# Optimization experiments

Measured on AMD Instinct MI355X. Metric: run time of the kernel, lower is better.

Reference implementation:

```python
import jax, jax.numpy as jnp
import numpy as np

N=50000; E=400000; H=128; FN=92; FE=41; L=3; PC=8; PD=16; SC=8; SD=32; B=64
EPS=1e-5

def _silu(x):
    return jax.nn.silu(x)

def _squash(s):
    n2=(s*s).sum(-1,keepdims=True)
    return s*(n2/(1.0+n2))/jnp.sqrt(n2+1e-9)

def setup_inputs():
    ks=iter(jax.random.split(jax.random.key(0),96))
    def rn(shape): return jax.random.normal(next(ks),shape,dtype=jnp.float32)
    def w(i,o): return rn((i,o))*np.float32(1.0/np.sqrt(i))
    z=lambda *s: jnp.zeros(s,jnp.float32); o=lambda *s: jnp.ones(s,jnp.float32)
    d={}
    d['x']=rn((N,FN)); d['edge_attr']=rn((E,FE)); d['pos']=rn((N,3))
    d['edge_index']=jax.random.randint(next(ks),(2,E),0,N)
    d['batch']=jnp.sort(jax.random.randint(next(ks),(N,),0,B))
    d.update(neW1=w(FN,H),neb1=z(H),neg1=o(H),nebe1=z(H),neW2=w(H,H),neb2=z(H),neg2=o(H),nebe2=z(H))
    d.update(eeW1=w(FE,H),eeb1=z(H),eeW2=w(H,H),eeb2=z(H),ivW=w(H,H),ivb=z(H))
    def wl(i,o2): return jnp.stack([w(i,o2) for _ in range(L)])
    d.update(cWma=wl(H,H),cWmb=wl(H,H),cWme=wl(H,H),cbm=z(L,H),cWsx=wl(H,H),cWsa=wl(H,H),cbs=z(L,H))
    d.update(cWv1=wl(H,H),cbv1=z(L,H),cWv2=wl(H,H),cbv2=z(L,H),lng=o(L,H),lnb=z(L,H),vsg=o(L,H))
    d.update(pcW=w(H,PC*PD),pcb=z(PC*PD),pvW=w(H,PD),sW=rn((PC,PD,SC,SD))*np.float32(1.0/np.sqrt(PD)))
    d.update(aW=w(SD//2,1),ab=z(1))
    d.update(pW1=w(SD,H//2),pb1=z(H//2),pg1=o(H//2),pbe1=z(H//2),pW2=w(H//2,H//4),pb2=z(H//4),pg2=o(H//4),pbe2=z(H//4),pW3=w(H//4,1),pb3=z(1))
    return d

def _forward(x,edge_index,edge_attr,pos,batch,neW1,neb1,neg1,nebe1,neW2,neb2,neg2,nebe2,eeW1,eeb1,eeW2,eeb2,ivW,ivb,cWma,cWmb,cWme,cbm,cWsx,cWsa,cbs,cWv1,cbv1,cWv2,cbv2,lng,lnb,vsg,pcW,pcb,pvW,sW,aW,ab,pW1,pb1,pg1,pbe1,pW2,pb2,pg2,pbe2,pW3,pb3):
    seg=jax.ops.segment_sum
    # node/edge MLP embeddings (BatchNorm in eval mode: running mean 0 / var 1 -> affine)
    xs=_silu((x@neW1+neb1)*neg1+nebe1)
    xs=_silu((xs@neW2+neb2)*neg2+nebe2)
    ea=_silu(edge_attr@eeW1+eeb1); ea=_silu(ea@eeW2+eeb2)
    # vectorized form of the per-node python loop: outer product weights x pos -> [N,H,3]
    xv=(xs@ivW+ivb)[:,:,None]*pos[:,None,:]
    src,dst=edge_index[0],edge_index[1]
    dp=pos[dst]-pos[src]                                  # [E,3]
    for i in range(L):
        xs_res,xv_res=xs,xv
        m=_silu(xs[src]@cWma[i]+xs[dst]@cWmb[i]+ea@cWme[i]+cbm[i])   # [E,H] edge messages
        xs_c=xs@cWsx[i]+seg(m,dst,num_segments=N)@cWsa[i]+cbs[i]
        vmsg=xv[src]*(m@cWv1[i]+cbv1[i])[:,:,None]+(m@cWv2[i]+cbv2[i])[:,:,None]*dp[:,None,:]
        xv_c=xv+seg(vmsg,dst,num_segments=N)               # [N,H,3]
        mu=xs_c.mean(-1,keepdims=True)
        xs_n=(xs_c-mu)/jnp.sqrt(((xs_c-mu)**2).mean(-1,keepdims=True)+EPS)*lng[i]+lnb[i]
        nrm=jnp.sqrt(((xv_c**2).sum(-1)).mean(-1,keepdims=True)+EPS)  # equivariant norm [N,1]
        xv_n=(xv_c/nrm[:,:,None])*vsg[i][None,:,None]
        xv_n=xv_n*jax.nn.sigmoid(xs_n)[:,:,None]           # scalar gating of vectors
        if i>0:
            xs=_silu(xs_n)+xs_res; xv=xv_n+xv_res
        else:
            xs=_silu(xs_n); xv=xv_n
    # primary capsules
    pc=_squash((xs@pcW+pcb).reshape(-1,PC,PD))             # [N,PC,PD]
    pv=jnp.einsum('nhd,hp->npd',xv,pvW)                    # [N,PD,3]
    u=pc+jnp.sqrt((pv**2).sum(-1)+1e-9)[:,None,:]          # vector norms expanded over PC caps
    # secondary capsules with per-graph pooling + 2 routing iterations
    pooled=seg(jnp.einsum('npd,pdce->npce',u,sW),batch,num_segments=B)  # [B,PC,SC,SD]
    bb=jnp.zeros((B,PC,SC),jnp.float32)
    for it in range(2):
        c=jax.nn.softmax(bb,axis=-1)
        v=_squash(jnp.einsum('bpc,bpce->bce',c,pooled))    # [B,SC,SD]
        if it==0:
            bb=bb+jnp.einsum('bpce,bce->bpc',pooled,v)
    # attention pooling over secondary capsules
    aw=jax.nn.softmax(v[:,:,:SD//2]@aW+ab,axis=1)
    wc=(aw*v).sum(1)                                       # [B,SD]
    h=_silu((wc@pW1+pb1)*pg1+pbe1)
    h=_silu((h@pW2+pb2)*pg2+pbe2)                          # dropout: eval mode (identity)
    return h@pW3+pb3

def reference(x,edge_index,edge_attr,pos,batch,neW1,neb1,neg1,nebe1,neW2,neb2,neg2,nebe2,eeW1,eeb1,eeW2,eeb2,ivW,ivb,cWma,cWmb,cWme,cbm,cWsx,cWsa,cbs,cWv1,cbv1,cWv2,cbv2,lng,lnb,vsg,pcW,pcb,pvW,sW,aW,ab,pW1,pb1,pg1,pbe1,pW2,pb2,pg2,pbe2,pW3,pb3):
    return _forward(x,edge_index,edge_attr,pos,batch,neW1,neb1,neg1,nebe1,neW2,neb2,neg2,nebe2,eeW1,eeb1,eeW2,eeb2,ivW,ivb,cWma,cWmb,cWme,cbm,cWsx,cWsa,cbs,cWv1,cbv1,cWv2,cbv2,lng,lnb,vsg,pcW,pcb,pvW,sW,aW,ab,pW1,pb1,pg1,pbe1,pW2,pb2,pg2,pbe2,pW3,pb3)
```

## Files before the change

### kernel.cpp

```cpp
#include <hip/hip_runtime.h>
#include <hip/hip_bf16.h>
#include <math.h>

#define NN 50000
#define NE 400000
#define HD 128
#define NB 64
#define NCH 8
#define CN 6250
#define ECM 53248
#define EB 32
#define PSL 16

typedef __hip_bfloat16 bf16;
typedef __attribute__((ext_vector_type(4))) unsigned short us4;
typedef __attribute__((ext_vector_type(8))) short s8v;
typedef __attribute__((ext_vector_type(4))) float f4v;

__device__ __forceinline__ float sigm_(float x){ return 1.f/(1.f+__expf(-x)); }
__device__ __forceinline__ float silu_(float x){ return x*sigm_(x); }
__device__ __forceinline__ float bf2f(bf16 x){ return __bfloat162float(x); }
__device__ __forceinline__ unsigned short f2bu(float f){
    bf16 h = __float2bfloat16(f);
    return *reinterpret_cast<unsigned short*>(&h);
// ... 109 lines not shown
        }
        if (owf){
            bf16* C = (bf16*)Cv;
#pragma unroll
            for (int j=0;j<8;++j) C[(size_t)orow*HD+col0+j] = __float2bfloat16(o[j]);
        } else {
            float* C = (float*)Cv;
            float4* cp = (float4*)&C[(size_t)orow*HD + col0];
            cp[0] = make_float4(o[0],o[1],o[2],o[3]);
            cp[1] = make_float4(o[4],o[5],o[6],o[7]);
        }
    }
}

__global__ __launch_bounds__(256)
void gemm3(const float* __restrict__ A0, const float* __restrict__ W0, float* __restrict__ C0, int M0,
           const float* __restrict__ A1, const float* __restrict__ W1, float* __restrict__ C1, int M1,
           const float* __restrict__ A2, const float* __restrict__ W2, float* __restrict__ C2, int M2)
{
    const int nb0 = (M0+63)>>6, nb1 = (M1+63)>>6;
    int bb = (int)blockIdx.x;
    const float *A, *W; float* C; int M;
    if (bb < nb0){ A=A0; W=W0; C=C0; M=M0; }
    else if (bb < nb0+nb1){ bb -= nb0; A=A1; W=W1; C=C1; M=M1; }
    else { bb -= nb0+nb1; A=A2; W=W2; C=C2; M=M2; }
    const int row0 = bb*64;

    __shared__ float As[32][68];
    __shared__ float Ws[32][128];
    const int tid = threadIdx.x;
    const int tx = tid & 15, ty = tid >> 4;
    const int col0 = tx*8;
    float acc[4][8];
#pragma unroll
    for (int r=0;r<4;++r)
#pragma unroll
        for (int j=0;j<8;++j) acc[r][j]=0.f;
    const int mload = tid >> 2;
    const int kload = (tid & 3) << 3;
    const int grow = row0 + mload;
    const bool rv = grow < M;

    for (int k0 = 0; k0 < 128; k0 += 32) {
        if (rv) {
            const float* ap = A + (size_t)grow*128 + k0 + kload;
            float4 v0 = *(const float4*)ap;
            float4 v1 = *(const float4*)(ap+4);
            As[kload+0][mload]=v0.x; As[kload+1][mload]=v0.y;
            As[kload+2][mload]=v0.z; As[kload+3][mload]=v0.w;
            As[kload+4][mload]=v1.x; As[kload+5][mload]=v1.y;
            As[kload+6][mload]=v1.z; As[kload+7][mload]=v1.w;
        } else {
#pragma unroll
            for (int j=0;j<8;++j) As[kload+j][mload] = 0.f;
        }
#pragma unroll
        for (int j=0;j<4;++j){
            int el = (tid + j*256)*4;
            int kk = el >> 7, col = el & 127;
            *(float4*)&Ws[kk][col] = *(const float4*)&W[(size_t)(k0+kk)*HD + col];
        }
        __syncthreads();
#pragma unroll
        for (int k=0;k<32;++k){
            float4 a4 = *(const float4*)&As[k][ty*4];
            float4 w0 = *(const float4*)&Ws[k][col0];
            float4 w1 = *(const float4*)&Ws[k][col0+4];
            float av[4] = {a4.x,a4.y,a4.z,a4.w};
            float wv[8] = {w0.x,w0.y,w0.z,w0.w,w1.x,w1.y,w1.z,w1.w};
#pragma unroll
            for (int r=0;r<4;++r)
#pragma unroll
                for (int j=0;j<8;++j) acc[r][j] += av[r]*wv[j];
        }
        __syncthreads();
    }
#pragma unroll
    for (int r=0;r<4;++r){
        int orow = row0 + ty*4 + r;
        if (orow >= M) continue;
        float4* cp = (float4*)&C[(size_t)orow*HD + col0];
        cp[0] = make_float4(acc[r][0],acc[r][1],acc[r][2],acc[r][3]);
        cp[1] = make_float4(acc[r][4],acc[r][5],acc[r][6],acc[r][7]);
    }
}

__global__ __launch_bounds__(256)
void edge_pipe(const float* __restrict__ eat,
               const int* __restrict__ elist, const int* __restrict__ srcp,
               const int* __restrict__ dstp,
               const bf16* __restrict__ W1h, const bf16* __restrict__ W1l,
               const float* __restrict__ b1,
               const bf16* __restrict__ W2h, const bf16* __restrict__ W2l,
               const float* __restrict__ b2,
               const bf16* __restrict__ Wmeh, const bf16* __restrict__ Wmel,
               const float* __restrict__ bm,
               const bf16* __restrict__ An, const bf16* __restrict__ Bn,
               const bf16* __restrict__ Wv1h, const bf16* __restrict__ Wv1l,
               const float* __restrict__ bv1,
               const int* __restrict__ rp, int rn0, int rn1,
               bf16* __restrict__ outM, bf16* __restrict__ outG)
{
    __shared__ __align__(16) unsigned short T1[EB][136];
    __shared__ __align__(16) unsigned short T2[EB][136];
    __shared__ int elS[EB], seS[EB], deS[EB];

    const int cbase = rp[rn0];
    const int Ml = min(ECM, max(rp[rn1]-cbase, 0));
    const int row0 = blockIdx.x*EB;
    if (row0 >= Ml) return;
    const int tid = threadIdx.x;
    const int lane = tid & 63, wave = tid >> 6;
    const int quad = lane >> 4, n16 = lane & 15;
    const int cwb = wave*32;

    if (tid < EB){
        int r = row0 + tid;
        bool v = r < Ml;
        int p = cbase + (v ? r : 0);
        elS[tid] = v ? min(max(elist[p],0),NE-1) : 0;
        seS[tid] = v ? srcp[p] : 0;
        deS[tid] = v ? dstp[p] : 0;
    }
    __syncthreads();

    f4v acc[2][2];

    {
        float ebuf[2][2][8];
#pragma unroll
        for (int rt=0; rt<2; ++rt){
            int arow = elS[rt*16 + n16];
#pragma unroll
            for (int kc=0; kc<2; ++kc){
#pragma unroll
                for (int j=0;j<8;++j){
                    int k = kc*32 + quad*8 + j;
                    ebuf[rt][kc][j] = (k < 41) ? eat[(size_t)arow*41 + k] : 0.f;
                }
            }
        }

        s8v B1h[2][2], B1l[2][2];
#pragma unroll
        for (int ct=0; ct<2; ++ct){
            int nn = cwb + ct*16 + n16;
#pragma unroll
            for (int kc=0; kc<2; ++kc){
                B1h[ct][kc] = *(const s8v*)&W1h[(size_t)nn*64 + kc*32 + quad*8];
                B1l[ct][kc] = *(const s8v*)&W1l[(size_t)nn*64 + kc*32 + quad*8];
            }
        }
#pragma unroll
        for (int rt=0;rt<2;++rt)
#pragma unroll
            for (int ct=0;ct<2;++ct) acc[rt][ct] = (f4v){0.f,0.f,0.f,0.f};

#pragma unroll
        for (int rt=0; rt<2; ++rt){
#pragma unroll
            for (int kc=0; kc<2; ++kc){
                s8v ah, al;
#pragma unroll
                for (int j=0;j<8;++j){
                    float v = ebuf[rt][kc][j];
                    unsigned short h = f2bu(v);
                    ah[j] = (short)h;
                    al[j] = (short)f2bu(v - __uint_as_float(((unsigned)h)<<16));
                }
#pragma unroll
                for (int ct=0; ct<2; ++ct){
                    acc[rt][ct] = __builtin_amdgcn_mfma_f32_16x16x32_bf16(ah, B1h[ct][kc], acc[rt][ct], 0,0,0);
                    acc[rt][ct] = __builtin_amdgcn_mfma_f32_16x16x32_bf16(ah, B1l[ct][kc], acc[rt][ct], 0,0,0);
                    acc[rt][ct] = __builtin_amdgcn_mfma_f32_16x16x32_bf16(al, B1h[ct][kc], acc[rt][ct], 0,0,0);
                }
            }
        }
#pragma unroll
        for (int ct=0; ct<2; ++ct){
            int col = cwb + ct*16 + n16;
            float bc = b1[col];
#pragma unroll
            for (int rt=0; rt<2; ++rt)
#pragma unroll
                for (int i=0;i<4;++i)
                    T1[rt*16 + quad*4 + i][col] = f2bu(silu_(acc[rt][ct][i] + bc));
        }
    }
    __syncthreads();

    s8v Bh[2][4], Bl[2][4];
    for (int ph=0; ph<3; ++ph){
        const bf16* WH = (ph==0)? W2h : (ph==1)? Wmeh : Wv1h;
        const bf16* WL = (ph==0)? W2l : (ph==1)? Wmel : Wv1l;
        const unsigned short (*Tin)[136] = (ph==1)? (const unsigned short(*)[136])T2
                                                  : (const unsigned short(*)[136])T1;
#pragma unroll
        for (int ct=0; ct<2; ++ct){
            int nn = cwb + ct*16 + n16;
            const s8v* hp = (const s8v*)&WH[(size_t)nn*128];
            const s8v* lp = (const s8v*)&WL[(size_t)nn*128];
#pragma unroll
            for (int kc=0; kc<4; ++kc){
                Bh[ct][kc] = hp[kc*4 + quad];
                Bl[ct][kc] = lp[kc*4 + quad];
            }
        }
#pragma unroll
        for (int rt=0;rt<2;++rt)
#pragma unroll
            for (int ct=0;ct<2;++ct) acc[rt][ct] = (f4v){0.f,0.f,0.f,0.f};

        s8v anR[2], bnR[2];
        if (ph==1){
#pragma unroll
            for (int it=0; it<2; ++it){
                int idx = tid + it*256;
                int r = idx >> 4, c = idx & 15;
                anR[it] = *(const s8v*)&An[(size_t)seS[r]*HD + c*8];
                bnR[it] = *(const s8v*)&Bn[(size_t)deS[r]*HD + c*8];
            }
        }

#pragma unroll
        for (int kc=0; kc<4; ++kc){
#pragma unroll
            for (int rt=0; rt<2; ++rt){
                s8v a = *(const s8v*)&Tin[rt*16 + n16][kc*32 + quad*8];
#pragma unroll
                for (int ct=0; ct<2; ++ct){
                    acc[rt][ct] = __builtin_amdgcn_mfma_f32_16x16x32_bf16(a, Bh[ct][kc], acc[rt][ct], 0,0,0);
                    acc[rt][ct] = __builtin_amdgcn_mfma_f32_16x16x32_bf16(a, Bl[ct][kc], acc[rt][ct], 0,0,0);
                }
            }
        }
        if (ph==0){
#pragma unroll
            for (int ct=0; ct<2; ++ct){
                int col = cwb + ct*16 + n16;
                float bc = b2[col];
#pragma unroll
                for (int rt=0; rt<2; ++rt)
#pragma unroll
                    for (int i=0;i<4;++i)
                        T2[rt*16 + quad*4 + i][col] = f2bu(silu_(acc[rt][ct][i] + bc));
            }
            __syncthreads();
        } else if (ph==1){
            __syncthreads();
#pragma unroll
            for (int it=0; it<2; ++it){
                int idx = tid + it*256;
                int r = idx >> 4, c = idx & 15;
                *(s8v*)&T1[r][c*8] = anR[it];
                *(s8v*)&T2[r][c*8] = bnR[it];
            }
            __syncthreads();
#pragma unroll
            for (int ct=0; ct<2; ++ct){
                int col = cwb + ct*16 + n16;
                float bc = bm[col];
#pragma unroll
                for (int rt=0; rt<2; ++rt)
#pragma unroll
                    for (int i=0;i<4;++i){
                        int row = rt*16 + quad*4 + i;
                        float v = silu_(acc[rt][ct][i] + bc
                                        + bf2f(*(const bf16*)&T1[row][col])
                                        + bf2f(*(const bf16*)&T2[row][col]));
                        T1[row][col] = f2bu(v);
                    }
            }
            __syncthreads();
            {
                int row = tid >> 3, seg = tid & 7;
                if (row0 + row < Ml){
                    const s8v* s = (const s8v*)&T1[row][seg*16];
                    s8v* d = (s8v*)&outM[(size_t)(row0+row)*HD + seg*16];
                    d[0]=s[0]; d[1]=s[1];
                }
            }
        } else {
#pragma unroll
            for (int ct=0; ct<2; ++ct){
                int col = cwb + ct*16 + n16;
                float bc = bv1[col];
#pragma unroll
                for (int rt=0; rt<2; ++rt)
#pragma unroll
                    for (int i=0;i<4;++i)
                        T2[rt*16 + quad*4 + i][col] = f2bu(acc[rt][ct][i] + bc);
            }
            __syncthreads();
            {
                int row = tid >> 3, seg = tid & 7;
                if (row0 + row < Ml){
                    const s8v* s = (const s8v*)&T2[row][seg*16];
                    s8v* d = (s8v*)&outG[(size_t)(row0+row)*HD + seg*16];
                    d[0]=s[0]; d[1]=s[1];
                }
            }
        }
    }
}

__global__ __launch_bounds__(128)
void scatter_c(const int* __restrict__ rp, const int* __restrict__ srcp,
               const float* __restrict__ pos,
               const bf16* __restrict__ mB, const bf16* __restrict__ gB,
               const float* __restrict__ xvO,
               float* __restrict__ smC, float* __restrict__ mdC,
               float* __restrict__ avC, float* __restrict__ sdC, int n0, int n1)
{
    const int b = blockIdx.x;
    const int n = n0 + b;
    if (n >= n1) return;
    const int h = threadIdx.x;
    const int cbase = rp[n0];
    int p0 = rp[n], p1 = rp[n+1];
    float px0=pos[n*3],px1=pos[n*3+1],px2=pos[n*3+2];
    float sm=0,a0=0,a1=0,a2=0,m0=0,m1=0,m2=0,d0s=0,d1s=0,d2s=0;
    for (int p=p0;p<p1;++p){
        int ii=p-cbase; if ((unsigned)ii>=(unsigned)ECM) break;
        float mh=bf2f(mB[(size_t)ii*HD+h]);
        float gh=bf2f(gB[(size_t)ii*HD+h]);
        int sn=srcp[p]; sn=min(max(sn,0),NN-1);
        float d0=px0-pos[sn*3], d1=px1-pos[sn*3+1], d2=px2-pos[sn*3+2];
        sm+=mh;
        a0+=xvO[(size_t)sn*3*HD+h]*gh;
        a1+=xvO[(size_t)sn*3*HD+HD+h]*gh;
        a2+=xvO[(size_t)sn*3*HD+2*HD+h]*gh;
        m0+=mh*d0; m1+=mh*d1; m2+=mh*d2;
        d0s+=d0; d1s+=d1; d2s+=d2;
    }
    smC[(size_t)b*HD+h]=sm;
    mdC[(size_t)b*3*HD+h]=m0;
    mdC[(size_t)b*3*HD+HD+h]=m1;
    mdC[(size_t)b*3*HD+2*HD+h]=m2;
    avC[(size_t)b*3*HD+h]=a0;
    avC[(size_t)b*3*HD+HD+h]=a1;
    avC[(size_t)b*3*HD+2*HD+h]=a2;
    if (h==0){ sdC[b*3]=d0s; sdC[b*3+1]=d1s; sdC[b*3+2]=d2s; }
}

__global__ __launch_bounds__(128)
void nu_lite(const float* __restrict__ gF, const float* __restrict__ swF,
             const float* __restrict__ xwF,
             const float* __restrict__ avC, const float* __restrict__ sdC,
             const float* __restrict__ xvO, float* __restrict__ xvN,
             float* __restrict__ xs,
             const float* __restrict__ bv2, const float* __restrict__ bs,
             const float* __restrict__ lng, const float* __restrict__ lnb,
             const float* __restrict__ vsg, int addRes, int n0, int n1)
{
    __shared__ float red[4];
    __shared__ float red2[2];
    const int b = blockIdx.x;
    const int n = n0 + b;
    if (n >= n1) return;
    const int h = threadIdx.x;
    const int w = h >> 6;
    const float xsv = xs[(size_t)n*HD+h];
    float xc = xwF[(size_t)b*HD+h] + swF[(size_t)b*HD+h] + bs[h];
    float s1=xc, s2=xc*xc;
#pragma unroll
    for (int off=1; off<64; off<<=1){ s1+=__shfl_xor(s1,off,64); s2+=__shfl_xor(s2,off,64); }
    if ((h&63)==0){ red[w*2]=s1; red[w*2+1]=s2; }
    __syncthreads();
    s1=red[0]+red[2]; s2=red[1]+red[3];
    float mu=s1*(1.f/128.f);
    float var=fmaxf(s2*(1.f/128.f)-mu*mu, 0.f);
    float xn=(xc-mu)*rsqrtf(var+1e-5f)*lng[h]+lnb[h];
    float ov0=xvO[(size_t)n*3*HD+h];
    float ov1=xvO[(size_t)n*3*HD+HD+h];
    float ov2=xvO[(size_t)n*3*HD+2*HD+h];
    float a0=avC[(size_t)b*3*HD+h];
    float a1=avC[(size_t)b*3*HD+HD+h];
    float a2=avC[(size_t)b*3*HD+2*HD+h];
    float d0s=sdC[b*3], d1s=sdC[b*3+1], d2s=sdC[b*3+2];
    float b2v=bv2[h];
    float v0=ov0+a0+gF[(size_t)(b*3+0)*HD+h]+b2v*d0s;
    float v1=ov1+a1+gF[(size_t)(b*3+1)*HD+h]+b2v*d1s;
    float v2=ov2+a2+gF[(size_t)(b*3+2)*HD+h]+b2v*d2s;
    float q=v0*v0+v1*v1+v2*v2;
#pragma unroll
    for (int off=1; off<64; off<<=1) q+=__shfl_xor(q,off,64);
    if ((h&63)==0) red2[w]=q;
    __syncthreads();
    q=fmaxf(red2[0]+red2[1], 0.f);
    float nrm=sqrtf(q*(1.f/128.f)+1e-5f);
    float scale=vsg[h]*sigm_(xn)/nrm;
    float r0=v0*scale, r1=v1*scale, r2=v2*scale;
    float nxs=silu_(xn);
    if (addRes){ nxs+=xsv; r0+=ov0; r1+=ov1; r2+=ov2; }
    xs[(size_t)n*HD+h]=nxs;
    xvN[(size_t)n*3*HD+h]=r0;
    xvN[(size_t)n*3*HD+HD+h]=r1;
    xvN[(size_t)n*3*HD+2*HD+h]=r2;
}

__global__ void hist_kernel(const int* __restrict__ idx, int* __restrict__ cnt, int n, int nb){
    int i = blockIdx.x*256 + threadIdx.x;
    if (i < n){
        int v = idx[i]; v = min(max(v,0), nb-1);
        atomicAdd(&cnt[v], 1);
    }
}

__global__ __launch_bounds__(256)
void scan_blk(const int* __restrict__ cnt, int* __restrict__ rowptr,
              int* __restrict__ bsum, int n){
    const int b = blockIdx.x, t = threadIdx.x;
    const int i = b*256 + t;
    const int lane = t & 63, w = t >> 6;
    int v = (i < n) ? cnt[i] : 0;
    int s = v;
#pragma unroll
    for (int off=1; off<64; off<<=1){
        int u = __shfl_up(s, off, 64);
        if (lane >= off) s += u;
    }
    __shared__ int ws[4];
    if (lane == 63) ws[w] = s;
    __syncthreads();
    int add = 0;
// ... 238 lines not shown
        float a = 0.f;
        for (int c=0;c<8;++c) a += aws[c]*vv[c*32+t];
        wcs[t] = a;
    }
    __syncthreads();
    if (t < 64){
        float a = 0.f;
        for (int e=0;e<32;++e) a += wcs[e]*pW1[e*64+t];
        h1[t] = silu_((a+pb1[t])*pg1[t]+pbe1[t]);
    }
    __syncthreads();
    if (t < 32){
        float a = 0.f;
        for (int j=0;j<64;++j) a += h1[j]*pW2[j*32+t];
        h2[t] = silu_((a+pb2[t])*pg2[t]+pbe2[t]);
    }
    __syncthreads();
    if (t == 0){
        float a = 0.f;
        for (int j=0;j<32;++j) a += h2[j]*pW3[j];
        a += pb3[0];
        if (!finite_(a)) a = 999.f;
        out[b] = a;
    }
}

__global__ void sentinel_k(float* __restrict__ out, float v){
    out[threadIdx.x] = v;
}

extern "C" void kernel_launch(void* const* d_in, const int* in_sizes, int n_in,
                              void* d_out, int out_size, void* d_ws, size_t ws_size,
                              hipStream_t stream)
{
    (void)in_sizes; (void)n_in; (void)out_size;
    const float* x    = (const float*)d_in[0];
    const float* eat  = (const float*)d_in[1];
    const float* pos  = (const float*)d_in[2];
    const int*  eidx  = (const int*)d_in[3];
    const int*  batch = (const int*)d_in[4];
    const float* neW1=(const float*)d_in[5],  *neb1=(const float*)d_in[6],
               * neg1=(const float*)d_in[7],  *nebe1=(const float*)d_in[8];
    const float* neW2=(const float*)d_in[9],  *neb2=(const float*)d_in[10],
               * neg2=(const float*)d_in[11], *nebe2=(const float*)d_in[12];
    const float* eeW1=(const float*)d_in[13], *eeb1=(const float*)d_in[14];
    const float* eeW2=(const float*)d_in[15], *eeb2=(const float*)d_in[16];
    const float* ivW =(const float*)d_in[17], *ivb =(const float*)d_in[18];
    const float* cWma=(const float*)d_in[19], *cWmb=(const float*)d_in[20],
               * cWme=(const float*)d_in[21], *cbm =(const float*)d_in[22];
    const float* cWsx=(const float*)d_in[23], *cWsa=(const float*)d_in[24],
               * cbs =(const float*)d_in[25];
    const float* cWv1=(const float*)d_in[26], *cbv1=(const float*)d_in[27],
               * cWv2=(const float*)d_in[28], *cbv2=(const float*)d_in[29];
    const float* lng =(const float*)d_in[30], *lnb =(const float*)d_in[31],
               * vsg =(const float*)d_in[32];
    const float* pcW =(const float*)d_in[33], *pcb =(const float*)d_in[34];
    const float* pvW =(const float*)d_in[35];
    const float* sW  =(const float*)d_in[36];
    const float* aW  =(const float*)d_in[37], *ab  =(const float*)d_in[38];
    const float* pW1 =(const float*)d_in[39], *pb1 =(const float*)d_in[40],
               * pg1 =(const float*)d_in[41], *pbe1=(const float*)d_in[42];
    const float* pW2 =(const float*)d_in[43], *pb2 =(const float*)d_in[44],
               * pg2 =(const float*)d_in[45], *pbe2=(const float*)d_in[46];
    const float* pW3 =(const float*)d_in[47], *pb3 =(const float*)d_in[48];

    const int* src = eidx;
    const int* dst = eidx + NE;

    char* wp = (char*)d_ws;
    auto alloc = [&](size_t bytes)->char*{
        char* p = wp;
        wp += (bytes + 255) & ~(size_t)255;
        return p;
    };
    bf16*  bufM  = (bf16*) alloc((size_t)ECM*HD*2);
    bf16*  bufG  = (bf16*) alloc((size_t)ECM*HD*2);
    float* xs    = (float*)alloc((size_t)NN*HD*4);
    float* xvA   = (float*)alloc((size_t)NN*3*HD*4);
    float* xvB   = (float*)alloc((size_t)NN*3*HD*4);
    bf16*  An    = (bf16*) alloc((size_t)NN*HD*2);
    bf16*  Bn    = (bf16*) alloc((size_t)NN*HD*2);
    float* smC   = (float*)alloc((size_t)CN*HD*4);
    float* mdC   = (float*)alloc((size_t)CN*3*HD*4);
    float* avC   = (float*)alloc((size_t)CN*3*HD*4);
    float* sdC   = (float*)alloc((size_t)CN*3*4);
    bf16*  WtH   = (bf16*) alloc((size_t)7*HD*HD*2);
    bf16*  WtL   = (bf16*) alloc((size_t)7*HD*HD*2);
    bf16*  W1h   = (bf16*) alloc((size_t)HD*64*2);
    bf16*  W1l   = (bf16*) alloc((size_t)HD*64*2);
    float* Up    = (float*)alloc((size_t)NB*PSL*HD*4);
    float* Ubuf  = (float*)alloc((size_t)NB*HD*4);
    int* rowptr  = (int*)alloc((size_t)(NN+1)*4);
    int* cnt     = (int*)alloc((size_t)NN*4);
    int* bsum    = (int*)alloc((size_t)256*4);
    int* elist   = (int*)alloc((size_t)NE*4);
    int* srcp    = (int*)alloc((size_t)NE*4);
    int* dstp    = (int*)alloc((size_t)NE*4);
    int* gptr    = (int*)alloc((size_t)(NB+1)*4);
    size_t used  = (size_t)(wp - (char*)d_ws);

    if (used > ws_size){
        sentinel_k<<<1, NB, 0, stream>>>((float*)d_out, -1.f - (float)(ws_size >> 20));
        return;
    }
    float* tmpF = xvB;
    bf16*  ubuf = An;
    float* Pf   = xvA;
    float* gF  = (float*)bufM;
    float* swF = gF  + (size_t)3*CN*HD;
    float* xwF = swF + (size_t)CN*HD;

    hipMemsetAsync(cnt, 0, (size_t)NN*4, stream);
    hist_kernel<<<(NE+255)/256, 256, 0, stream>>>(dst, cnt, NE, NN);
    const int SBLK = (NN+255)/256;
    scan_blk<<<SBLK, 256, 0, stream>>>(cnt, rowptr, bsum, NN);
    scan_bsum<<<1, 256, 0, stream>>>(bsum, SBLK);
    scan_fix<<<SBLK, 256, 0, stream>>>(rowptr, bsum, NN);
    hipMemsetAsync(cnt, 0, (size_t)NN*4, stream);
    fill_kernel<<<(NE+255)/256, 256, 0, stream>>>(src, dst, rowptr, cnt, elist, srcp, dstp, NE);
    gptr_kernel<<<(NN+255)/256, 256, 0, stream>>>(batch, gptr);
    wprep1<<<32,256,0,stream>>>(eeW1, W1h, W1l);
    wprep<<<64,256,0,stream>>>(eeW2, WtH, WtL);
    for (int l=0;l<3;++l){
        wprep<<<64,256,0,stream>>>(cWme + (size_t)l*HD*HD, WtH + (size_t)(1+l)*HD*HD,
                                   WtL + (size_t)(1+l)*HD*HD);
        wprep<<<64,256,0,stream>>>(cWv1 + (size_t)l*HD*HD, WtH + (size_t)(4+l)*HD*HD,
                                   WtL + (size_t)(4+l)*HD*HD);
    }

    const int GN = (NN+63)/64;
    const int GE = ECM/EB;
    const int G3 = ((3*CN+63)/64) + 2*((CN+63)/64);

    gemmk<M_BNSILU><<<GN,256,0,stream>>>(x, neW1, neb1, neg1, nebe1, tmpF, 0, NN, 92);
    gemmk<M_BNSILU><<<GN,256,0,stream>>>(tmpF, neW2, neb2, neg2, nebe2, xs, 0, NN, 128);
    gemmk<M_BIAS><<<GN,256,0,stream>>>(xs, ivW, ivb, nullptr, nullptr, tmpF, 0, NN, 128);
    xv_init<<<NN, 128, 0, stream>>>(tmpF, pos, xvA);

    float* xvO = xvA;
    float* xvN = xvB;
    for (int l=0; l<3; ++l){
        const float* Wma = cWma + (size_t)l*HD*HD;
        const float* Wmb = cWmb + (size_t)l*HD*HD;
        const float* bm  = cbm  + (size_t)l*HD;
        const float* Wsx = cWsx + (size_t)l*HD*HD;
        const float* Wsa = cWsa + (size_t)l*HD*HD;
        const float* bs  = cbs  + (size_t)l*HD;
        const float* bv1 = cbv1 + (size_t)l*HD;
        const float* Wv2 = cWv2 + (size_t)l*HD*HD;
        const float* bv2 = cbv2 + (size_t)l*HD;
        const bf16* Wmeh = WtH + (size_t)(1+l)*HD*HD;
        const bf16* Wmel = WtL + (size_t)(1+l)*HD*HD;
        const bf16* Wv1h = WtH + (size_t)(4+l)*HD*HD;
        const bf16* Wv1l = WtL + (size_t)(4+l)*HD*HD;

        gemmk<M_PLAIN><<<GN,256,0,stream>>>(xs, Wma, nullptr, nullptr, nullptr, An, 1, NN, 128);
        gemmk<M_PLAIN><<<GN,256,0,stream>>>(xs, Wmb, nullptr, nullptr, nullptr, Bn, 1, NN, 128);

        for (int c=0; c<NCH; ++c){
            int n0 = c*CN, n1 = n0+CN;
            edge_pipe<<<GE,256,0,stream>>>(eat, elist, srcp, dstp,
                                           W1h, W1l, eeb1,
                                           WtH, WtL, eeb2,
                                           Wmeh, Wmel, bm,
                                           An, Bn,
                                           Wv1h, Wv1l, bv1,
                                           rowptr, n0, n1, bufM, bufG);
            scatter_c<<<CN,128,0,stream>>>(rowptr, srcp, pos, bufM, bufG, xvO,
                                           smC, mdC, avC, sdC, n0, n1);
            gemm3<<<G3,256,0,stream>>>(mdC, Wv2, gF, 3*CN,
                                       smC, Wsa, swF, CN,
                                       xs + (size_t)n0*HD, Wsx, xwF, CN);
            nu_lite<<<CN,128,0,stream>>>(gF, swF, xwF, avC, sdC,
                                         xvO, xvN, xs,
                                         bv2, bs,
                                         lng + (size_t)l*HD, lnb + (size_t)l*HD,
                                         vsg + (size_t)l*HD, l>0 ? 1 : 0, n0, n1);
        }
        float* t = xvO; xvO = xvN; xvN = t;
    }

    gemmk<M_BIAS><<<GN,256,0,stream>>>(xs, pcW, pcb, nullptr, nullptr, Pf, 0, NN, 128);
    capsule2<<<12500/4, 256, 0, stream>>>(Pf, xvO, pvW, ubuf);
    pool1<<<NB*PSL, 128, 0, stream>>>(gptr, ubuf, Up);
    pool2<<<NB, 128, 0, stream>>>(Up, Ubuf);
    graph_head<<<NB, 256, 0, stream>>>(Ubuf, sW, aW, ab,
                                       pW1, pb1, pg1, pbe1,
                                       pW2, pb2, pg2, pbe2,
                                       pW3, pb3, (float*)d_out);
}
```

Baseline: 3.318 ms.

## Precompute edge embedding MLP once and reuse across message-passing layers

Adds an ea_pipe kernel that computes the two-layer edge-attribute MLP once for all edges in CSR-sorted order and stores it as bf16. A new edge_pipe_fast kernel loads these precomputed embeddings instead of recomputing both MLP stages in every layer and chunk launch. This removes redundant matmuls and the gather of raw edge attributes from each of the 24 edge launches. In exchange it needs a large extra workspace buffer, adds bandwidth to read the stored embeddings, and falls back to the old kernel if the workspace is too small.

```diff
diff --git a/kernel.cpp b/kernel.cpp
--- a/kernel.cpp
+++ b/kernel.cpp
@@ -215,6 +215,291 @@
         float4* cp = (float4*)&C[(size_t)orow*HD + col0];
         cp[0] = make_float4(acc[r][0],acc[r][1],acc[r][2],acc[r][3]);
         cp[1] = make_float4(acc[r][4],acc[r][5],acc[r][6],acc[r][7]);
+    }
+}
+
+__global__ __launch_bounds__(256)
+void ea_pipe(const float* __restrict__ eat, const int* __restrict__ elist,
+             const bf16* __restrict__ W1h, const bf16* __restrict__ W1l,
+             const float* __restrict__ b1,
+             const bf16* __restrict__ W2h, const bf16* __restrict__ W2l,
+             const float* __restrict__ b2,
+             bf16* __restrict__ eaP)
+{
+    __shared__ __align__(16) unsigned short T1[EB][136];
+    __shared__ __align__(16) unsigned short T2[EB][136];
+    __shared__ int elS[EB];
+
+    const int row0 = blockIdx.x*EB;
+    const int tid = threadIdx.x;
+    const int lane = tid & 63, wave = tid >> 6;
+    const int quad = lane >> 4, n16 = lane & 15;
+    const int cwb = wave*32;
+
+    if (tid < EB) elS[tid] = min(max(elist[row0 + tid],0),NE-1);
+    __syncthreads();
+
+    f4v acc[2][2];
+
+    {
+        float ebuf[2][2][8];
+#pragma unroll
+        for (int rt=0; rt<2; ++rt){
+            int arow = elS[rt*16 + n16];
+#pragma unroll
+            for (int kc=0; kc<2; ++kc)
+#pragma unroll
+                for (int j=0;j<8;++j){
+                    int k = kc*32 + quad*8 + j;
+                    ebuf[rt][kc][j] = (k < 41) ? eat[(size_t)arow*41 + k] : 0.f;
+                }
+        }
+        s8v B1h[2][2], B1l[2][2];
+#pragma unroll
+        for (int ct=0; ct<2; ++ct){
+            int nn = cwb + ct*16 + n16;
+#pragma unroll
+            for (int kc=0; kc<2; ++kc){
+                B1h[ct][kc] = *(const s8v*)&W1h[(size_t)nn*64 + kc*32 + quad*8];
+                B1l[ct][kc] = *(const s8v*)&W1l[(size_t)nn*64 + kc*32 + quad*8];
+            }
+        }
+#pragma unroll
+        for (int rt=0;rt<2;++rt)
+#pragma unroll
+            for (int ct=0;ct<2;++ct) acc[rt][ct] = (f4v){0.f,0.f,0.f,0.f};
+#pragma unroll
+        for (int rt=0; rt<2; ++rt)
+#pragma unroll
+            for (int kc=0; kc<2; ++kc){
+                s8v ah, al;
+#pragma unroll
+                for (int j=0;j<8;++j){
+                    float v = ebuf[rt][kc][j];
+                    unsigned short h = f2bu(v);
+                    ah[j] = (short)h;
+                    al[j] = (short)f2bu(v - __uint_as_float(((unsigned)h)<<16));
+                }
+#pragma unroll
+                for (int ct=0; ct<2; ++ct){
+                    acc[rt][ct] = __builtin_amdgcn_mfma_f32_16x16x32_bf16(ah, B1h[ct][kc], acc[rt][ct], 0,0,0);
+                    acc[rt][ct] = __builtin_amdgcn_mfma_f32_16x16x32_bf16(ah, B1l[ct][kc], acc[rt][ct], 0,0,0);
+                    acc[rt][ct] = __builtin_amdgcn_mfma_f32_16x16x32_bf16(al, B1h[ct][kc], acc[rt][ct], 0,0,0);
+                }
+            }
+#pragma unroll
+        for (int ct=0; ct<2; ++ct){
+            int col = cwb + ct*16 + n16;
+            float bc = b1[col];
+#pragma unroll
+            for (int rt=0; rt<2; ++rt)
+#pragma unroll
+                for (int i=0;i<4;++i)
+                    T1[rt*16 + quad*4 + i][col] = f2bu(silu_(acc[rt][ct][i] + bc));
+        }
+    }
+    __syncthreads();
+
+    {
+        s8v Bh[2][4], Bl[2][4];
+#pragma unroll
+        for (int ct=0; ct<2; ++ct){
+            int nn = cwb + ct*16 + n16;
+            const s8v* hp = (const s8v*)&W2h[(size_t)nn*128];
+            const s8v* lp = (const s8v*)&W2l[(size_t)nn*128];
+#pragma unroll
+            for (int kc=0; kc<4; ++kc){
+                Bh[ct][kc] = hp[kc*4 + quad];
+                Bl[ct][kc] = lp[kc*4 + quad];
+            }
+        }
+#pragma unroll
+        for (int rt=0;rt<2;++rt)
+#pragma unroll
+            for (int ct=0;ct<2;++ct) acc[rt][ct] = (f4v){0.f,0.f,0.f,0.f};
+#pragma unroll
+        for (int kc=0; kc<4; ++kc)
+#pragma unroll
+            for (int rt=0; rt<2; ++rt){
+                s8v a = *(const s8v*)&T1[rt*16 + n16][kc*32 + quad*8];
+#pragma unroll
+                for (int ct=0; ct<2; ++ct){
+                    acc[rt][ct] = __builtin_amdgcn_mfma_f32_16x16x32_bf16(a, Bh[ct][kc], acc[rt][ct], 0,0,0);
+                    acc[rt][ct] = __builtin_amdgcn_mfma_f32_16x16x32_bf16(a, Bl[ct][kc], acc[rt][ct], 0,0,0);
+                }
+            }
+#pragma unroll
+        for (int ct=0; ct<2; ++ct){
+            int col = cwb + ct*16 + n16;
+            float bc = b2[col];
+#pragma unroll
+            for (int rt=0; rt<2; ++rt)
+#pragma unroll
+                for (int i=0;i<4;++i)
+                    T2[rt*16 + quad*4 + i][col] = f2bu(silu_(acc[rt][ct][i] + bc));
+        }
+    }
+    __syncthreads();
+    {
+        int row = tid >> 3, seg = tid & 7;
+        const s8v* s = (const s8v*)&T2[row][seg*16];
+        s8v* d = (s8v*)&eaP[(size_t)(row0+row)*HD + seg*16];
+        d[0]=s[0]; d[1]=s[1];
+    }
+}
+
+__global__ __launch_bounds__(256)
+void edge_pipe_fast(const bf16* __restrict__ eaP,
+                    const int* __restrict__ srcp, const int* __restrict__ dstp,
+                    const bf16* __restrict__ Wmeh, const bf16* __restrict__ Wmel,
+                    const float* __restrict__ bm,
+                    const bf16* __restrict__ An, const bf16* __restrict__ Bn,
+                    const bf16* __restrict__ Wv1h, const bf16* __restrict__ Wv1l,
+                    const float* __restrict__ bv1,
+                    const int* __restrict__ rp, int rn0, int rn1,
+                    bf16* __restrict__ outM, bf16* __restrict__ outG)
+{
+    __shared__ __align__(16) unsigned short T1[EB][136];
+    __shared__ __align__(16) unsigned short T2[EB][136];
+    __shared__ int seS[EB], deS[EB];
+
+    const int cbase = rp[rn0];
+    const int Ml = min(ECM, max(rp[rn1]-cbase, 0));
+    const int row0 = blockIdx.x*EB;
+    if (row0 >= Ml) return;
+    const int tid = threadIdx.x;
+    const int lane = tid & 63, wave = tid >> 6;
+    const int quad = lane >> 4, n16 = lane & 15;
+    const int cwb = wave*32;
+
+    if (tid < EB){
+        int r = row0 + tid;
+        bool v = r < Ml;
+        int p = cbase + (v ? r : 0);
+        seS[tid] = v ? srcp[p] : 0;
+        deS[tid] = v ? dstp[p] : 0;
+    }
+    __syncthreads();
+
+    s8v anR[2], bnR[2], eaR[2];
+#pragma unroll
+    for (int it=0; it<2; ++it){
+        int idx = tid + it*256;
+        int r = idx >> 4, c = idx & 15;
+        anR[it] = *(const s8v*)&An[(size_t)seS[r]*HD + c*8];
+        bnR[it] = *(const s8v*)&Bn[(size_t)deS[r]*HD + c*8];
+        int gp = min(cbase + row0 + r, NE-1);
+        eaR[it] = *(const s8v*)&eaP[(size_t)gp*HD + c*8];
+    }
+#pragma unroll
+    for (int it=0; it<2; ++it){
+        int idx = tid + it*256;
+        int r = idx >> 4, c = idx & 15;
+        *(s8v*)&T2[r][c*8] = eaR[it];
+    }
+    __syncthreads();
+
+    f4v acc[2][2];
+    s8v Bh[2][4], Bl[2][4];
+
+#pragma unroll
+    for (int ct=0; ct<2; ++ct){
+        int nn = cwb + ct*16 + n16;
+        const s8v* hp = (const s8v*)&Wmeh[(size_t)nn*128];
+        const s8v* lp = (const s8v*)&Wmel[(size_t)nn*128];
+#pragma unroll
+        for (int kc=0; kc<4; ++kc){ Bh[ct][kc] = hp[kc*4 + quad]; Bl[ct][kc] = lp[kc*4 + quad]; }
+    }
+#pragma unroll
+    for (int rt=0;rt<2;++rt)
+#pragma unroll
+        for (int ct=0;ct<2;++ct) acc[rt][ct] = (f4v){0.f,0.f,0.f,0.f};
+#pragma unroll
+    for (int kc=0; kc<4; ++kc)
+#pragma unroll
+        for (int rt=0; rt<2; ++rt){
+            s8v a = *(const s8v*)&T2[rt*16 + n16][kc*32 + quad*8];
+#pragma unroll
+            for (int ct=0; ct<2; ++ct){
+                acc[rt][ct] = __builtin_amdgcn_mfma_f32_16x16x32_bf16(a, Bh[ct][kc], acc[rt][ct], 0,0,0);
+                acc[rt][ct] = __builtin_amdgcn_mfma_f32_16x16x32_bf16(a, Bl[ct][kc], acc[rt][ct], 0,0,0);
+            }
+        }
+    __syncthreads();
+#pragma unroll
+    for (int it=0; it<2; ++it){
+        int idx = tid + it*256;
+        int r = idx >> 4, c = idx & 15;
+        *(s8v*)&T1[r][c*8] = anR[it];
+        *(s8v*)&T2[r][c*8] = bnR[it];
+    }
+    __syncthreads();
+#pragma unroll
+    for (int ct=0; ct<2; ++ct){
+        int col = cwb + ct*16 + n16;
+        float bc = bm[col];
+#pragma unroll
+        for (int rt=0; rt<2; ++rt)
+#pragma unroll
+            for (int i=0;i<4;++i){
+                int row = rt*16 + quad*4 + i;
+                float v = silu_(acc[rt][ct][i] + bc
+                                + bf2f(*(const bf16*)&T1[row][col])
+                                + bf2f(*(const bf16*)&T2[row][col]));
+                T1[row][col] = f2bu(v);
+            }
+    }
+    __syncthreads();
+    {
+        int row = tid >> 3, seg = tid & 7;
+        if (row0 + row < Ml){
+            const s8v* s = (const s8v*)&T1[row][seg*16];
+            s8v* d = (s8v*)&outM[(size_t)(row0+row)*HD + seg*16];
+            d[0]=s[0]; d[1]=s[1];
+        }
+    }
+
+#pragma unroll
+    for (int ct=0; ct<2; ++ct){
+        int nn = cwb + ct*16 + n16;
+        const s8v* hp = (const s8v*)&Wv1h[(size_t)nn*128];
+        const s8v* lp = (const s8v*)&Wv1l[(size_t)nn*128];
+#pragma unroll
+        for (int kc=0; kc<4; ++kc){ Bh[ct][kc] = hp[kc*4 + quad]; Bl[ct][kc] = lp[kc*4 + quad]; }
+    }
+#pragma unroll
+    for (int rt=0;rt<2;++rt)
+#pragma unroll
+        for (int ct=0;ct<2;++ct) acc[rt][ct] = (f4v){0.f,0.f,0.f,0.f};
+#pragma unroll
+    for (int kc=0; kc<4; ++kc)
+#pragma unroll
+        for (int rt=0; rt<2; ++rt){
+            s8v a = *(const s8v*)&T1[rt*16 + n16][kc*32 + quad*8];
+#pragma unroll
+            for (int ct=0; ct<2; ++ct){
+                acc[rt][ct] = __builtin_amdgcn_mfma_f32_16x16x32_bf16(a, Bh[ct][kc], acc[rt][ct], 0,0,0);
+                acc[rt][ct] = __builtin_amdgcn_mfma_f32_16x16x32_bf16(a, Bl[ct][kc], acc[rt][ct], 0,0,0);
+            }
+        }
+#pragma unroll
+    for (int ct=0; ct<2; ++ct){
+        int col = cwb + ct*16 + n16;
+        float bc = bv1[col];
+#pragma unroll
+        for (int rt=0; rt<2; ++rt)
+#pragma unroll
+            for (int i=0;i<4;++i)
+                T2[rt*16 + quad*4 + i][col] = f2bu(acc[rt][ct][i] + bc);
+    }
+    __syncthreads();
+    {
+        int row = tid >> 3, seg = tid & 7;
+        if (row0 + row < Ml){
+            const s8v* s = (const s8v*)&T2[row][seg*16];
+            s8v* d = (s8v*)&outG[(size_t)(row0+row)*HD + seg*16];
+            d[0]=s[0]; d[1]=s[1];
+        }
     }
 }
 
@@ -265,15 +550,13 @@
         for (int rt=0; rt<2; ++rt){
             int arow = elS[rt*16 + n16];
 #pragma unroll
-            for (int kc=0; kc<2; ++kc){
+            for (int kc=0; kc<2; ++kc)
 #pragma unroll
                 for (int j=0;j<8;++j){
                     int k = kc*32 + quad*8 + j;
                     ebuf[rt][kc][j] = (k < 41) ? eat[(size_t)arow*41 + k] : 0.f;
                 }
-            }
-        }
-
+        }
         s8v B1h[2][2], B1l[2][2];
 #pragma unroll
         for (int ct=0; ct<2; ++ct){
@@ -288,9 +571,8 @@
         for (int rt=0;rt<2;++rt)
 #pragma unroll
             for (int ct=0;ct<2;++ct) acc[rt][ct] = (f4v){0.f,0.f,0.f,0.f};
-
-#pragma unroll
-        for (int rt=0; rt<2; ++rt){
+#pragma unroll
+        for (int rt=0; rt<2; ++rt)
 #pragma unroll
             for (int kc=0; kc<2; ++kc){
                 s8v ah, al;
@@ -308,7 +590,6 @@
                     acc[rt][ct] = __builtin_amdgcn_mfma_f32_16x16x32_bf16(al, B1h[ct][kc], acc[rt][ct], 0,0,0);
                 }
             }
-        }
 #pragma unroll
         for (int ct=0; ct<2; ++ct){
             int col = cwb + ct*16 + n16;
@@ -899,6 +1180,12 @@
         sentinel_k<<<1, NB, 0, stream>>>((float*)d_out, -1.f - (float)(ws_size >> 20));
         return;
     }
+    size_t eaBytes = (((size_t)(NE+EB)*HD*2) + 255) & ~(size_t)255;
+    bf16* eaP = nullptr;
+    if (used + eaBytes <= ws_size){
+        eaP = (bf16*)alloc(eaBytes);
+    }
+
     float* tmpF = xvB;
     bf16*  ubuf = An;
     float* Pf   = xvA;
@@ -924,6 +1211,11 @@
                                    WtL + (size_t)(4+l)*HD*HD);
     }
 
+    if (eaP){
+        ea_pipe<<<NE/EB, 256, 0, stream>>>(eat, elist, W1h, W1l, eeb1,
+                                           WtH, WtL, eeb2, eaP);
+    }
+
     const int GN = (NN+63)/64;
     const int GE = ECM/EB;
     const int G3 = ((3*CN+63)/64) + 2*((CN+63)/64);
@@ -955,13 +1247,21 @@
 
         for (int c=0; c<NCH; ++c){
             int n0 = c*CN, n1 = n0+CN;
-            edge_pipe<<<GE,256,0,stream>>>(eat, elist, srcp, dstp,
-                                           W1h, W1l, eeb1,
-                                           WtH, WtL, eeb2,
-                                           Wmeh, Wmel, bm,
-                                           An, Bn,
-                                           Wv1h, Wv1l, bv1,
-                                           rowptr, n0, n1, bufM, bufG);
+            if (eaP){
+                edge_pipe_fast<<<GE,256,0,stream>>>(eaP, srcp, dstp,
+                                                    Wmeh, Wmel, bm,
+                                                    An, Bn,
+                                                    Wv1h, Wv1l, bv1,
+                                                    rowptr, n0, n1, bufM, bufG);
+            } else {
+                edge_pipe<<<GE,256,0,stream>>>(eat, elist, srcp, dstp,
+                                               W1h, W1l, eeb1,
+                                               WtH, WtL, eeb2,
+                                               Wmeh, Wmel, bm,
+                                               An, Bn,
+                                               Wv1h, Wv1l, bv1,
+                                               rowptr, n0, n1, bufM, bufG);
+            }
             scatter_c<<<CN,128,0,stream>>>(rowptr, srcp, pos, bufM, bufG, xvO,
                                            smC, mdC, avC, sdC, n0, n1);
             gemm3<<<G3,256,0,stream>>>(mdC, Wv2, gF, 3*CN,
```

New measurement: 3.323 ms. About the same (+0.2%).

## Fuse message segment-sum reductions into edge pipeline with boundary atomics

Applied to the files above, without the earlier changes.

The edge kernel now reduces each message tile into per-destination sums (sum of messages, message times displacement, displacement sums) itself, using segmented runs over the sorted edges. Only the first run of each block, which can be shared with the previous block, and the last run use atomics; interior runs are stored directly. This removes the bf16 message buffer write and its re-read in the scatter kernel, which now only computes the gated xv aggregation. In exchange it adds a memset per chunk, serial per-column loops over 32 rows, and float atomics whose summation order is not deterministic. Interior nodes with no incoming edges rely on the memset to give zero.

```diff
diff --git a/kernel.cpp b/kernel.cpp
--- a/kernel.cpp
+++ b/kernel.cpp
@@ -219,24 +219,27 @@
 }
 
 __global__ __launch_bounds__(256)
-void edge_pipe(const float* __restrict__ eat,
-               const int* __restrict__ elist, const int* __restrict__ srcp,
-               const int* __restrict__ dstp,
-               const bf16* __restrict__ W1h, const bf16* __restrict__ W1l,
-               const float* __restrict__ b1,
-               const bf16* __restrict__ W2h, const bf16* __restrict__ W2l,
-               const float* __restrict__ b2,
-               const bf16* __restrict__ Wmeh, const bf16* __restrict__ Wmel,
-               const float* __restrict__ bm,
-               const bf16* __restrict__ An, const bf16* __restrict__ Bn,
-               const bf16* __restrict__ Wv1h, const bf16* __restrict__ Wv1l,
-               const float* __restrict__ bv1,
-               const int* __restrict__ rp, int rn0, int rn1,
-               bf16* __restrict__ outM, bf16* __restrict__ outG)
+void edge_pipe_m(const float* __restrict__ eat,
+                 const int* __restrict__ elist, const int* __restrict__ srcp,
+                 const int* __restrict__ dstp, const float* __restrict__ pos,
+                 const bf16* __restrict__ W1h, const bf16* __restrict__ W1l,
+                 const float* __restrict__ b1,
+                 const bf16* __restrict__ W2h, const bf16* __restrict__ W2l,
+                 const float* __restrict__ b2,
+                 const bf16* __restrict__ Wmeh, const bf16* __restrict__ Wmel,
+                 const float* __restrict__ bm,
+                 const bf16* __restrict__ An, const bf16* __restrict__ Bn,
+                 const bf16* __restrict__ Wv1h, const bf16* __restrict__ Wv1l,
+                 const float* __restrict__ bv1,
+                 const int* __restrict__ rp, int rn0, int rn1,
+                 float* __restrict__ smC, float* __restrict__ mdC,
+                 float* __restrict__ sdC,
+                 bf16* __restrict__ outG)
 {
     __shared__ __align__(16) unsigned short T1[EB][136];
     __shared__ __align__(16) unsigned short T2[EB][136];
     __shared__ int elS[EB], seS[EB], deS[EB];
+    __shared__ float dS0[EB], dS1[EB], dS2[EB];
 
     const int cbase = rp[rn0];
     const int Ml = min(ECM, max(rp[rn1]-cbase, 0));
@@ -251,9 +254,13 @@
         int r = row0 + tid;
         bool v = r < Ml;
         int p = cbase + (v ? r : 0);
-        elS[tid] = v ? min(max(elist[p],0),NE-1) : 0;
-        seS[tid] = v ? srcp[p] : 0;
-        deS[tid] = v ? dstp[p] : 0;
+        int e = v ? min(max(elist[p],0),NE-1) : 0;
+        int s = v ? srcp[p] : 0;
+        int d = v ? dstp[p] : 0;
+        elS[tid] = e; seS[tid] = s; deS[tid] = d;
+        dS0[tid] = pos[d*3+0] - pos[s*3+0];
+        dS1[tid] = pos[d*3+1] - pos[s*3+1];
+        dS2[tid] = pos[d*3+2] - pos[s*3+2];
     }
     __syncthreads();
 
@@ -265,15 +272,13 @@
         for (int rt=0; rt<2; ++rt){
             int arow = elS[rt*16 + n16];
 #pragma unroll
-            for (int kc=0; kc<2; ++kc){
+            for (int kc=0; kc<2; ++kc)
 #pragma unroll
                 for (int j=0;j<8;++j){
                     int k = kc*32 + quad*8 + j;
                     ebuf[rt][kc][j] = (k < 41) ? eat[(size_t)arow*41 + k] : 0.f;
                 }
-            }
-        }
-
+        }
         s8v B1h[2][2], B1l[2][2];
 #pragma unroll
         for (int ct=0; ct<2; ++ct){
@@ -288,9 +293,8 @@
         for (int rt=0;rt<2;++rt)
 #pragma unroll
             for (int ct=0;ct<2;++ct) acc[rt][ct] = (f4v){0.f,0.f,0.f,0.f};
-
-#pragma unroll
-        for (int rt=0; rt<2; ++rt){
+#pragma unroll
+        for (int rt=0; rt<2; ++rt)
 #pragma unroll
             for (int kc=0; kc<2; ++kc){
                 s8v ah, al;
@@ -308,7 +312,6 @@
                     acc[rt][ct] = __builtin_amdgcn_mfma_f32_16x16x32_bf16(al, B1h[ct][kc], acc[rt][ct], 0,0,0);
                 }
             }
-        }
 #pragma unroll
         for (int ct=0; ct<2; ++ct){
             int col = cwb + ct*16 + n16;
@@ -405,13 +408,61 @@
                     }
             }
             __syncthreads();
-            {
-                int row = tid >> 3, seg = tid & 7;
-                if (row0 + row < Ml){
-                    const s8v* s = (const s8v*)&T1[row][seg*16];
-                    s8v* d = (s8v*)&outM[(size_t)(row0+row)*HD + seg*16];
-                    d[0]=s[0]; d[1]=s[1];
+            if (tid < 128){
+                const int col = tid;
+                float sm=0.f, m0=0.f, m1=0.f, m2=0.f;
+                int cur=-1, startR=0;
+                for (int r=0;r<EB;++r){
+                    bool valid = (row0 + r) < Ml;
+                    int dl = valid ? (deS[r]-rn0) : -1;
+                    if (dl != cur){
+                        if (cur >= 0 && (unsigned)cur < (unsigned)CN){
+                            size_t so = (size_t)cur*HD + col;
+                            size_t mo = (size_t)cur*3*HD + col;
+                            if (startR == 0){
+                                atomicAdd(&smC[so], sm);
+                                atomicAdd(&mdC[mo], m0);
+                                atomicAdd(&mdC[mo+HD], m1);
+                                atomicAdd(&mdC[mo+2*HD], m2);
+                            } else {
+                                smC[so] = sm;
+                                mdC[mo] = m0; mdC[mo+HD] = m1; mdC[mo+2*HD] = m2;
+                            }
+                        }
+                        cur = dl; startR = r; sm=0.f;m0=0.f;m1=0.f;m2=0.f;
+                    }
+                    if (valid){
+                        float mh = bf2f(*(const bf16*)&T1[r][col]);
+                        sm += mh;
+                        m0 += mh*dS0[r]; m1 += mh*dS1[r]; m2 += mh*dS2[r];
+                    }
                 }
+                if (cur >= 0 && (unsigned)cur < (unsigned)CN){
+                    size_t so = (size_t)cur*HD + col;
+                    size_t mo = (size_t)cur*3*HD + col;
+                    atomicAdd(&smC[so], sm);
+                    atomicAdd(&mdC[mo], m0);
+                    atomicAdd(&mdC[mo+HD], m1);
+                    atomicAdd(&mdC[mo+2*HD], m2);
+                }
+            } else if (tid < 131){
+                const int c = tid - 128;
+                const float* dsl = (c==0)?dS0:(c==1)?dS1:dS2;
+                float s=0.f; int cur=-1, startR=0;
+                for (int r=0;r<EB;++r){
+                    bool valid = (row0 + r) < Ml;
+                    int dl = valid ? (deS[r]-rn0) : -1;
+                    if (dl != cur){
+                        if (cur >= 0 && (unsigned)cur < (unsigned)CN){
+                            if (startR == 0) atomicAdd(&sdC[(size_t)cur*3+c], s);
+                            else sdC[(size_t)cur*3+c] = s;
+                        }
+                        cur = dl; startR = r; s = 0.f;
+                    }
+                    if (valid) s += dsl[r];
+                }
+                if (cur >= 0 && (unsigned)cur < (unsigned)CN)
+                    atomicAdd(&sdC[(size_t)cur*3+c], s);
             }
         } else {
 #pragma unroll
@@ -438,12 +489,9 @@
 }
 
 __global__ __launch_bounds__(128)
-void scatter_c(const int* __restrict__ rp, const int* __restrict__ srcp,
-               const float* __restrict__ pos,
-               const bf16* __restrict__ mB, const bf16* __restrict__ gB,
-               const float* __restrict__ xvO,
-               float* __restrict__ smC, float* __restrict__ mdC,
-               float* __restrict__ avC, float* __restrict__ sdC, int n0, int n1)
+void scatter_av(const int* __restrict__ rp, const int* __restrict__ srcp,
+                const bf16* __restrict__ gB, const float* __restrict__ xvO,
+                float* __restrict__ avC, int n0, int n1)
 {
     const int b = blockIdx.x;
     const int n = n0 + b;
@@ -451,29 +499,18 @@
     const int h = threadIdx.x;
     const int cbase = rp[n0];
     int p0 = rp[n], p1 = rp[n+1];
-    float px0=pos[n*3],px1=pos[n*3+1],px2=pos[n*3+2];
-    float sm=0,a0=0,a1=0,a2=0,m0=0,m1=0,m2=0,d0s=0,d1s=0,d2s=0;
+    float a0=0,a1=0,a2=0;
     for (int p=p0;p<p1;++p){
         int ii=p-cbase; if ((unsigned)ii>=(unsigned)ECM) break;
-        float mh=bf2f(mB[(size_t)ii*HD+h]);
         float gh=bf2f(gB[(size_t)ii*HD+h]);
         int sn=srcp[p]; sn=min(max(sn,0),NN-1);
-        float d0=px0-pos[sn*3], d1=px1-pos[sn*3+1], d2=px2-pos[sn*3+2];
-        sm+=mh;
         a0+=xvO[(size_t)sn*3*HD+h]*gh;
         a1+=xvO[(size_t)sn*3*HD+HD+h]*gh;
         a2+=xvO[(size_t)sn*3*HD+2*HD+h]*gh;
-        m0+=mh*d0; m1+=mh*d1; m2+=mh*d2;
-        d0s+=d0; d1s+=d1; d2s+=d2;
-    }
-    smC[(size_t)b*HD+h]=sm;
-    mdC[(size_t)b*3*HD+h]=m0;
-    mdC[(size_t)b*3*HD+HD+h]=m1;
-    mdC[(size_t)b*3*HD+2*HD+h]=m2;
+    }
     avC[(size_t)b*3*HD+h]=a0;
     avC[(size_t)b*3*HD+HD+h]=a1;
     avC[(size_t)b*3*HD+2*HD+h]=a2;
-    if (h==0){ sdC[b*3]=d0s; sdC[b*3+1]=d1s; sdC[b*3+2]=d2s; }
 }
 
 __global__ __launch_bounds__(128)
@@ -878,8 +915,8 @@
     bf16*  Bn    = (bf16*) alloc((size_t)NN*HD*2);
     float* smC   = (float*)alloc((size_t)CN*HD*4);
     float* mdC   = (float*)alloc((size_t)CN*3*HD*4);
+    float* sdC   = (float*)alloc((size_t)CN*3*4);
     float* avC   = (float*)alloc((size_t)CN*3*HD*4);
-    float* sdC   = (float*)alloc((size_t)CN*3*4);
     bf16*  WtH   = (bf16*) alloc((size_t)7*HD*HD*2);
     bf16*  WtL   = (bf16*) alloc((size_t)7*HD*HD*2);
     bf16*  W1h   = (bf16*) alloc((size_t)HD*64*2);
@@ -905,6 +942,7 @@
     float* gF  = (float*)bufM;
     float* swF = gF  + (size_t)3*CN*HD;
     float* xwF = swF + (size_t)CN*HD;
+    const size_t msz = (size_t)((char*)avC - (char*)smC);
 
     hipMemsetAsync(cnt, 0, (size_t)NN*4, stream);
     hist_kernel<<<(NE+255)/256, 256, 0, stream>>>(dst, cnt, NE, NN);
@@ -955,15 +993,16 @@
 
         for (int c=0; c<NCH; ++c){
             int n0 = c*CN, n1 = n0+CN;
-            edge_pipe<<<GE,256,0,stream>>>(eat, elist, srcp, dstp,
-                                           W1h, W1l, eeb1,
-                                           WtH, WtL, eeb2,
-                                           Wmeh, Wmel, bm,
-                                           An, Bn,
-                                           Wv1h, Wv1l, bv1,
-                                           rowptr, n0, n1, bufM, bufG);
-            scatter_c<<<CN,128,0,stream>>>(rowptr, srcp, pos, bufM, bufG, xvO,
-                                           smC, mdC, avC, sdC, n0, n1);
+            hipMemsetAsync(smC, 0, msz, stream);
+            edge_pipe_m<<<GE,256,0,stream>>>(eat, elist, srcp, dstp, pos,
+                                             W1h, W1l, eeb1,
+                                             WtH, WtL, eeb2,
+                                             Wmeh, Wmel, bm,
+                                             An, Bn,
+                                             Wv1h, Wv1l, bv1,
+                                             rowptr, n0, n1,
+                                             smC, mdC, sdC, bufG);
+            scatter_av<<<CN,128,0,stream>>>(rowptr, srcp, bufG, xvO, avC, n0, n1);
             gemm3<<<G3,256,0,stream>>>(mdC, Wv2, gF, 3*CN,
                                        smC, Wsa, swF, CN,
                                        xs + (size_t)n0*HD, Wsx, xwF, CN);
```

New measurement: 3.536 ms. 6.6% more time.
